# Optimization experiments

Measured on AMD Instinct MI355X. Metric: run time of the kernel, lower is better.

The kernel has to match this reference:

```python
import math
import jax, jax.numpy as jnp
import numpy as np

DIM = 384
NUM_HEADS = 12
KS = 7
GROUP_WIDTH = 8
LAM = 1.0
GAMMA = 1.0
DIM_QK = DIM // 3 * 2  # 256, multiple of group_width
DIM_V = DIM
SCALE = (DIM // NUM_HEADS) ** -0.5
GROUPS = DIM_QK // GROUP_WIDTH  # 32


def setup_inputs() -> dict:
    key = jax.random.key(0)
    ks = jax.random.split(key, 10)
    B_, N = 32, 196
    x = jax.random.normal(ks[0], (B_, N, DIM), dtype=jnp.float32)
    qkv_out = DIM_QK * 2 + DIM_V  # 704
    w_qkv = jax.random.normal(ks[1], (qkv_out, DIM), dtype=jnp.float32) * 0.02
    b_qkv = jnp.zeros((qkv_out,), dtype=jnp.float32)
    # grouped 7x7 conv: (out=DIM_QK, in_per_group=GROUP_WIDTH, KS, KS)
    w_dw = jax.random.normal(ks[2], (DIM_QK, GROUP_WIDTH, KS, KS), dtype=jnp.float32) * 0.05
    b_dw = jnp.zeros((DIM_QK,), dtype=jnp.float32)
    # 1x1 conv to KS^2 * num_heads channels
    w_pw = jax.random.normal(ks[3], (KS * KS * NUM_HEADS, DIM_QK), dtype=jnp.float32) * 0.05
    b_pw = jnp.zeros((KS * KS * NUM_HEADS,), dtype=jnp.float32)
    # ghost head: cat(ghost_mul ~ randn, ghost_add ~ trunc_normal(0.02)) -> (2,1,DIM_V,KS,KS)
    ghost_mul = jax.random.normal(ks[4], (1, 1, DIM_V, KS, KS), dtype=jnp.float32)
    ghost_add = jax.random.normal(ks[5], (1, 1, DIM_V, KS, KS), dtype=jnp.float32) * 0.02
    ghost_head = jnp.concatenate((ghost_mul, ghost_add), axis=0)
    w_proj = jax.random.normal(ks[6], (DIM, DIM_V), dtype=jnp.float32) * 0.02
    b_proj = jnp.zeros((DIM,), dtype=jnp.float32)
    return {"x": x, "w_qkv": w_qkv, "b_qkv": b_qkv, "w_dw": w_dw, "b_dw": b_dw,
            "w_pw": w_pw, "b_pw": b_pw, "ghost_head": ghost_head,
            "w_proj": w_proj, "b_proj": b_proj}


def reference(x, w_qkv, b_qkv, w_dw, b_dw, w_pw, b_pw, ghost_head, w_proj, b_proj):
    B, N, C = x.shape
    H = W = int(math.sqrt(N))
    G, Cg, ks = NUM_HEADS, DIM_V // NUM_HEADS, KS

    qkv = jnp.einsum('bnc,oc->bno', x, w_qkv) + b_qkv
    q, k, v = jnp.split(qkv, (DIM_QK, 2 * DIM_QK), axis=-1)
    q = jnp.transpose(q, (0, 2, 1)).reshape(B, DIM_QK, H, W)
    k = jnp.transpose(k, (0, 2, 1)).reshape(B, DIM_QK, H, W)
    v = jnp.transpose(v, (0, 2, 1)).reshape(B, DIM_V, H, W)

    # Hadamard QK interaction + attention-map generator
    hp = q * k * SCALE
    pad = ks // 2
    h = jax.lax.conv_general_dilated(
        hp, w_dw, window_strides=(1, 1), padding=((pad, pad), (pad, pad)),
        feature_group_count=GROUPS, dimension_numbers=('NCHW', 'OIHW', 'NCHW'))
    h = h + b_dw[None, :, None, None]
    h = jax.nn.gelu(h, approximate=False)
    h = jnp.einsum('bchw,oc->bohw', h, w_pw) + b_pw[None, :, None, None]  # (B, ks^2*G, H, W)

    h_attn = jax.nn.softmax(h.reshape(B * G, ks * ks, H, W), axis=1)
    v_g = v.reshape(B * G, Cg, H, W)

    # ghost heads (broadcast over batch, split channels into heads)
    gh = jnp.broadcast_to(ghost_head, (2, B, DIM_V, ks, ks)).reshape(2, B * G, Cg, ks * ks)
    ghost_mul = gh[0] ** LAM        # (BG, Cg, ks^2)
    ghost_add = gh[1] * GAMMA       # (BG, Cg, ks^2)

    # elsa_op: windowed weighted sum (unfold equivalent, torch channel-major order)
    vp = jnp.pad(v_g, ((0, 0), (0, 0), (pad, pad), (pad, pad)))
    patches = jnp.stack([vp[:, :, i:i + H, j:j + W]
                         for i in range(ks) for j in range(ks)], axis=2)  # (BG, Cg, ks^2, H, W)
    filt = (ghost_mul[:, :, :, None, None] * h_attn[:, None, :, :, :]
            + ghost_add[:, :, :, None, None])
    out = (patches * filt).sum(axis=2)  # (BG, Cg, H, W)

    out = out.reshape(B, DIM_V, H, W).transpose(0, 2, 3, 1).reshape(B, N, DIM_V)
    y = jnp.einsum('bnc,oc->bno', out, w_proj) + b_proj
    return y
```

## Files before the change

### kernel.cpp

```cpp
#include <hip/hip_runtime.h>
#include <hip/hip_bf16.h>

#define B_    32
#define N_    196
#define H_    14
#define DIMC  384
#define DQK   256
#define DV    384
#define NH    12
#define CG    32
#define NPW   588
#define PAD_  3
#define SCALE_ 0.17677669529663687f

typedef __bf16 bf16x8 __attribute__((ext_vector_type(8)));
typedef float  f32x4  __attribute__((ext_vector_type(4)));

__device__ inline bf16x8 bf16x8_zero() {
    bf16x8 z;
    #pragma unroll
    for (int j = 0; j < 8; ++j) z[j] = (__bf16)0.0f;
    return z;
}

__device__ inline void split2(float v, __hip_bfloat16& h, __hip_bfloat16& l) {
    h = __float2bfloat16(v);
    l = __float2bfloat16(v - __bfloat162float(h));
}

__global__ __launch_bounds__(256) void k_split(
    const float* __restrict__ s0, const float* __restrict__ s1,
    const float* __restrict__ s2, const float* __restrict__ s3,
    __hip_bfloat16* __restrict__ h0, __hip_bfloat16* __restrict__ l0,
    __hip_bfloat16* __restrict__ h1, __hip_bfloat16* __restrict__ l1,
    __hip_bfloat16* __restrict__ h2, __hip_bfloat16* __restrict__ l2,
    __hip_bfloat16* __restrict__ h3, __hip_bfloat16* __restrict__ l3)
{
    int i = blockIdx.x * 256 + threadIdx.x;
    if (i >= 762624) return;
    const float* src; __hip_bfloat16 *dh, *dl; int off;
    if      (i < 602112) { src = s0; dh = h0; dl = l0; off = i; }
    else if (i < 688128) { src = s1; dh = h1; dl = l1; off = i - 602112; }
    else if (i < 725760) { src = s2; dh = h2; dl = l2; off = i - 688128; }
    else                 { src = s3; dh = h3; dl = l3; off = i - 725760; }
    const float4 v = ((const float4*)src)[off];
    union { __hip_bfloat16 b[4]; uint2 u; } H, L;
    split2(v.x, H.b[0], L.b[0]); split2(v.y, H.b[1], L.b[1]);
    split2(v.z, H.b[2], L.b[2]); split2(v.w, H.b[3], L.b[3]);
    ((uint2*)dh)[off] = H.u;
    ((uint2*)dl)[off] = L.u;
}

template<int EPI>
__global__ __launch_bounds__(256) void k_mfma(
    const __hip_bfloat16* __restrict__ Phi, const __hip_bfloat16* __restrict__ Plo,
    const __hip_bfloat16* __restrict__ Qhi, const __hip_bfloat16* __restrict__ Qlo,
    const float* __restrict__ bias, int K, int nQ,
    float* __restrict__ out0, float* __restrict__ out1, float* __restrict__ out2)
{
    __shared__ ushort lds[16384];
    const int t    = threadIdx.x;
    const int m0   = blockIdx.x * 128;
    const int n0   = blockIdx.y * 128;
    const int lane = t & 63;
    const int wv   = t >> 6;
    const int wm   = (wv >> 1) * 64;
    const int wn   = (wv & 1) * 64;
    const int l16  = lane & 15;
    const int kb   = lane >> 4;

    f32x4 acc[4][4];
    #pragma unroll
    for (int mi = 0; mi < 4; ++mi)
        #pragma unroll
        for (int nj = 0; nj < 4; ++nj) acc[mi][nj] = f32x4{0.f, 0.f, 0.f, 0.f};

    for (int k0 = 0; k0 < K; k0 += 32) {
        bf16x8 rA[2][2], rB[2][2];
        #pragma unroll
        for (int q = 0; q < 2; ++q) {
            const int u = q * 256 + t;
            const int r = u >> 2;
            const int kk = (u & 3) * 8;
            const size_t pOff = (size_t)(m0 + r) * K + k0 + kk;
            rA[q][0] = *(const bf16x8*)(Phi + pOff);
            rA[q][1] = *(const bf16x8*)(Plo + pOff);
            if (n0 + r < nQ) {
                const size_t qOff = (size_t)(n0 + r) * K + k0 + kk;
                rB[q][0] = *(const bf16x8*)(Qhi + qOff);
                rB[q][1] = *(const bf16x8*)(Qlo + qOff);
            } else { rB[q][0] = bf16x8_zero(); rB[q][1] = bf16x8_zero(); }
        }
        __syncthreads();
        #pragma unroll
        for (int q = 0; q < 2; ++q) {
            const int u  = q * 256 + t;
            const int r  = u >> 2;
            const int sw = ((u << 4) ^ ((r & 7) << 4)) >> 1;
            *(bf16x8*)&lds[sw]         = rA[q][0];
            *(bf16x8*)&lds[sw + 4096]  = rA[q][1];
            *(bf16x8*)&lds[sw + 8192]  = rB[q][0];
            *(bf16x8*)&lds[sw + 12288] = rB[q][1];
        }
        __syncthreads();
        bf16x8 bh[4], bl[4];
        #pragma unroll
        for (int nj = 0; nj < 4; ++nj) {
            const int br  = wn + nj * 16 + l16;
            const int idx = ((br * 64 + kb * 16) ^ ((br & 7) << 4)) >> 1;
            bh[nj] = *(const bf16x8*)&lds[8192 + idx];
            bl[nj] = *(const bf16x8*)&lds[12288 + idx];
        }
        #pragma unroll
        for (int mi = 0; mi < 4; ++mi) {
            const int ar  = wm + mi * 16 + l16;
            const int idx = ((ar * 64 + kb * 16) ^ ((ar & 7) << 4)) >> 1;
            const bf16x8 ah = *(const bf16x8*)&lds[idx];
            const bf16x8 al = *(const bf16x8*)&lds[4096 + idx];
            #pragma unroll
            for (int nj = 0; nj < 4; ++nj) {
                acc[mi][nj] = __builtin_amdgcn_mfma_f32_16x16x32_bf16(ah, bh[nj], acc[mi][nj], 0, 0, 0);
                acc[mi][nj] = __builtin_amdgcn_mfma_f32_16x16x32_bf16(ah, bl[nj], acc[mi][nj], 0, 0, 0);
                acc[mi][nj] = __builtin_amdgcn_mfma_f32_16x16x32_bf16(al, bh[nj], acc[mi][nj], 0, 0, 0);
            }
        }
    }

    #pragma unroll
    for (int mi = 0; mi < 4; ++mi) {
        #pragma unroll
        for (int r = 0; r < 4; ++r) {
            const int m = m0 + wm + mi * 16 + kb * 4 + r;
            #pragma unroll
            for (int nj = 0; nj < 4; ++nj) {
                const int col = n0 + wn + nj * 16 + l16;
                const float v = acc[mi][nj][r];
                if (EPI == 0) {
                    const float val = v + bias[col];
                    const int bb = m / N_, n = m - bb * N_;
                    if (col < DQK)          out0[((size_t)bb * DQK + col) * N_ + n] = val;
                    else if (col < 2*DQK)   out1[((size_t)bb * DQK + (col - DQK)) * N_ + n] = val;
                    else                    out2[((size_t)bb * DV + (col - 2*DQK)) * N_ + n] = val;
                } else if (EPI == 1) {
                    if (col < NPW) out0[(size_t)m * NPW + col] = v + bias[col];
                } else {
                    out0[(size_t)m * DV + col] = v + bias[col];
                }
            }
        }
    }
}

__global__ __launch_bounds__(256) void k_dwconv(const float* __restrict__ qT,
    const float* __restrict__ kT, const float* __restrict__ w_dw,
    const float* __restrict__ b_dw,
    __hip_bfloat16* __restrict__ h1t_hi, __hip_bfloat16* __restrict__ h1t_lo)
{
    const int b  = blockIdx.x;
    const int gp = blockIdx.y;
    __shared__ float hp[16 * 400];
    __shared__ float wsm[16 * 392];
    const int t = threadIdx.x;
    for (int i = t; i < 16 * 400; i += 256) hp[i] = 0.f;
    for (int i = t; i < 16 * 392; i += 256) wsm[i] = w_dw[gp * 6272 + i];
    __syncthreads();
    for (int i = t; i < 16 * N_; i += 256) {
        const int cl = i / N_;
        const int n  = i - cl * N_;
        const int y  = n / H_, x = n - y * H_;
        const size_t gi = ((size_t)b * DQK + gp * 16 + cl) * N_ + n;
        hp[cl * 400 + (y + PAD_) * 20 + (x + PAD_)] = qT[gi] * kT[gi] * SCALE_;
    }
    __syncthreads();
    if (t < 224) {
        const int od = t / 14;
        const int y  = t - od * 14;
        const int icb = (od >> 3) << 3;
        float acc[14];
        #pragma unroll
        for (int x = 0; x < 14; ++x) acc[x] = 0.f;
        for (int ic = 0; ic < 8; ++ic) {
            const float* hrow = &hp[(icb + ic) * 400];
            const float* wrow = &wsm[od * 392 + ic * 49];
            #pragma unroll
            for (int ky = 0; ky < 7; ++ky) {
                float r[20];
                #pragma unroll
                for (int ii = 0; ii < 20; ii += 4)
                    *(float4*)&r[ii] = *(const float4*)&hrow[(y + ky) * 20 + ii];
                #pragma unroll
                for (int kx = 0; kx < 7; ++kx) {
                    const float wv = wrow[ky * 7 + kx];
                    #pragma unroll
                    for (int x = 0; x < 14; ++x)
                        acc[x] += r[x + kx] * wv;
                }
            }
        }
        const float bv = b_dw[gp * 16 + od];
        const int c = gp * 16 + od;
        #pragma unroll
        for (int x = 0; x < 14; ++x) {
            const float s  = acc[x] + bv;
            const float gv = 0.5f * s * (1.f + erff(s * 0.70710678118654752440f));
            __hip_bfloat16 hb, lb; split2(gv, hb, lb);
            const size_t o = ((size_t)b * N_ + y * H_ + x) * DQK + c;
            h1t_hi[o] = hb; h1t_lo[o] = lb;
        }
    }
}

__global__ __launch_bounds__(256) void k_elsa(const float* __restrict__ h2t,
    const float* __restrict__ vT, const float* __restrict__ ghost,
    __hip_bfloat16* __restrict__ orm_hi, __hip_bfloat16* __restrict__ orm_lo)
{
    const int b = blockIdx.x;
    const int g = blockIdx.y;
    __shared__ float attn[49 * N_];
    __shared__ float vp[8 * 401];
    __shared__ float gm[8 * 49];
    __shared__ float ga[8 * 49];
    const int t = threadIdx.x;

    const float* src = h2t + (size_t)b * N_ * NPW + g * 49;
    for (int i = t; i < 49 * N_; i += 256) {
        const int n = i / 49, p = i - n * 49;
        attn[p * N_ + n] = src[(size_t)n * NPW + p];
    }
    __syncthreads();

    if (t < N_) {
        float mx = -1e30f;
        for (int p = 0; p < 49; ++p) mx = fmaxf(mx, attn[p * N_ + t]);
        float s = 0.f;
        for (int p = 0; p < 49; ++p) {
            const float e = expf(attn[p * N_ + t] - mx);
            attn[p * N_ + t] = e;
            s += e;
        }
        const float inv = 1.f / s;
        for (int p = 0; p < 49; ++p) attn[p * N_ + t] *= inv;
    }
    __syncthreads();

    for (int cc = 0; cc < 4; ++cc) {
        const int c0 = cc * 8;
        for (int i = t; i < 8 * 401; i += 256) vp[i] = 0.f;
        for (int i = t; i < 8 * 49; i += 256) {
            gm[i] = ghost[(size_t)(g * CG + c0) * 49 + i];
            ga[i] = ghost[(size_t)DV * 49 + (g * CG + c0) * 49 + i];
        }
        __syncthreads();
        for (int i = t; i < 8 * N_; i += 256) {
            const int c = i / N_;
            const int n = i - c * N_;
            const int y = n / H_, x = n - y * H_;
            vp[c * 401 + (y + PAD_) * 20 + (x + PAD_)] =
                vT[((size_t)b * DV + g * CG + c0 + c) * N_ + n];
        }
        __syncthreads();

        for (int idx = t; idx < 8 * N_; idx += 256) {
            const int c = idx & 7;
            const int n = idx >> 3;
            const int y = n / H_, x = n - y * H_;
            const float* vrow = &vp[c * 401];
            const float* gmr  = &gm[c * 49];
            const float* gar  = &ga[c * 49];
            float s = 0.f;
            #pragma unroll
            for (int ky = 0; ky < 7; ++ky)
                #pragma unroll
                for (int kx = 0; kx < 7; ++kx) {
                    const int p = ky * 7 + kx;
                    s += vrow[(y + ky) * 20 + (x + kx)]
                       * (gmr[p] * attn[p * N_ + n] + gar[p]);
                }
            __hip_bfloat16 hb, lb; split2(s, hb, lb);
            const size_t o = ((size_t)b * N_ + n) * DV + g * CG + c0 + c;
            orm_hi[o] = hb; orm_lo[o] = lb;
        }
        __syncthreads();
    }
}

extern "C" void kernel_launch(void* const* d_in, const int* in_sizes, int n_in,
                              void* d_out, int out_size, void* d_ws, size_t ws_size,
                              hipStream_t stream)
{
    const float* x      = (const float*)d_in[0];
    const float* w_qkv  = (const float*)d_in[1];
    const float* b_qkv  = (const float*)d_in[2];
    const float* w_dw   = (const float*)d_in[3];
    const float* b_dw   = (const float*)d_in[4];
    const float* w_pw   = (const float*)d_in[5];
    const float* b_pw   = (const float*)d_in[6];
    const float* ghost  = (const float*)d_in[7];
    const float* w_proj = (const float*)d_in[8];
    const float* b_proj = (const float*)d_in[9];
    float* y  = (float*)d_out;
    char* ws = (char*)d_ws;

    __hip_bfloat16* x_hi     = (__hip_bfloat16*)(ws + 0);
    __hip_bfloat16* x_lo     = (__hip_bfloat16*)(ws + 4816896);
    __hip_bfloat16* wqkv_hi  = (__hip_bfloat16*)(ws + 9633792);
    __hip_bfloat16* wqkv_lo  = (__hip_bfloat16*)(ws + 10321920);
    float*          h2t      = (float*)         (ws + 0);
    float*          qT       = (float*)         (ws + 14751744);
    float*          kT       = (float*)         (ws + 21174272);
    __hip_bfloat16* orm_hi   = (__hip_bfloat16*)(ws + 14751744);
    __hip_bfloat16* orm_lo   = (__hip_bfloat16*)(ws + 19568640);
    float*          vT       = (float*)         (ws + 27596800);
    __hip_bfloat16* wpw_hi   = (__hip_bfloat16*)(ws + 37230592);
    __hip_bfloat16* wpw_lo   = (__hip_bfloat16*)(ws + 37531648);
    __hip_bfloat16* wproj_hi = (__hip_bfloat16*)(ws + 37832704);
    __hip_bfloat16* wproj_lo = (__hip_bfloat16*)(ws + 38127616);
    __hip_bfloat16* h1t_hi   = (__hip_bfloat16*)(ws + 38422528);
    __hip_bfloat16* h1t_lo   = (__hip_bfloat16*)(ws + 41633792);

    k_split<<<2979, 256, 0, stream>>>(x, w_qkv, w_pw, w_proj,
        x_hi, x_lo, wqkv_hi, wqkv_lo, wpw_hi, wpw_lo, wproj_hi, wproj_lo);

    k_mfma<0><<<dim3(49, 7), 256, 0, stream>>>(x_hi, x_lo, wqkv_hi, wqkv_lo,
        b_qkv, DIMC, 896, qT, kT, vT);

    k_dwconv<<<dim3(32, 16), 256, 0, stream>>>(qT, kT, w_dw, b_dw, h1t_hi, h1t_lo);

    k_mfma<1><<<dim3(49, 5), 256, 0, stream>>>(h1t_hi, h1t_lo, wpw_hi, wpw_lo,
        b_pw, DQK, NPW, h2t, nullptr, nullptr);

    k_elsa<<<dim3(32, 12), 256, 0, stream>>>(h2t, vT, ghost, orm_hi, orm_lo);

    k_mfma<2><<<dim3(49, 3), 256, 0, stream>>>(orm_hi, orm_lo, wproj_hi, wproj_lo,
        b_proj, DV, DV, y, nullptr, nullptr);
}
```

Measured before the change: 260.0 us.

## Split ELSA kernel across channel chunks and keep softmax attention in registers

The ELSA kernel is now launched with a third grid dimension over the four 8-channel chunks, so four times as many blocks run and each handles only one chunk. Every thread owns one spatial position, loads its 49 attention logits straight from global memory, runs the softmax in registers and reuses those values across the 8 channels. This drops the large shared-memory attention transpose and several barriers, which should raise occupancy. The cost is that the softmax is recomputed once per chunk, each thread needs many more registers, and 60 of 256 threads sit idle.

Result: faster. 241.9 us (-7.0%).

```diff
diff --git a/kernel.cpp b/kernel.cpp
--- a/kernel.cpp
+++ b/kernel.cpp
@@ -214,73 +214,65 @@
     const float* __restrict__ vT, const float* __restrict__ ghost,
     __hip_bfloat16* __restrict__ orm_hi, __hip_bfloat16* __restrict__ orm_lo)
 {
-    const int b = blockIdx.x;
-    const int g = blockIdx.y;
-    __shared__ float attn[49 * N_];
-    __shared__ float vp[8 * 401];
-    __shared__ float gm[8 * 49];
-    __shared__ float ga[8 * 49];
+    const int b  = blockIdx.x;
+    const int g  = blockIdx.y;
+    const int c0 = blockIdx.z * 8;
+    __shared__ float vp[8 * 400];
+    __shared__ float gmga[8 * 49 * 2];
     const int t = threadIdx.x;
 
-    const float* src = h2t + (size_t)b * N_ * NPW + g * 49;
-    for (int i = t; i < 49 * N_; i += 256) {
-        const int n = i / 49, p = i - n * 49;
-        attn[p * N_ + n] = src[(size_t)n * NPW + p];
+    for (int i = t; i < 8 * 400; i += 256) vp[i] = 0.f;
+    for (int i = t; i < 8 * 49; i += 256) {
+        const int c = i / 49, p = i - c * 49;
+        gmga[(c * 49 + p) * 2 + 0] = ghost[(size_t)(g * CG + c0 + c) * 49 + p];
+        gmga[(c * 49 + p) * 2 + 1] = ghost[(size_t)DV * 49 + (g * CG + c0 + c) * 49 + p];
     }
     __syncthreads();
+    for (int i = t; i < 8 * N_; i += 256) {
+        const int c = i / N_;
+        const int n = i - c * N_;
+        const int y = n / H_, x = n - y * H_;
+        vp[c * 400 + (y + PAD_) * 20 + (x + PAD_)] =
+            vT[((size_t)b * DV + g * CG + c0 + c) * N_ + n];
+    }
+    __syncthreads();
 
     if (t < N_) {
+        const int n = t;
+        const int y = n / H_, x = n - y * H_;
+        const int base = y * 20 + x;
+        const size_t m = (size_t)b * N_ + n;
+
+        const float* hr = h2t + m * NPW + g * 49;
+        float a[49];
+        #pragma unroll
+        for (int p = 0; p < 49; ++p) a[p] = hr[p];
         float mx = -1e30f;
-        for (int p = 0; p < 49; ++p) mx = fmaxf(mx, attn[p * N_ + t]);
-        float s = 0.f;
-        for (int p = 0; p < 49; ++p) {
-            const float e = expf(attn[p * N_ + t] - mx);
-            attn[p * N_ + t] = e;
-            s += e;
-        }
-        const float inv = 1.f / s;
-        for (int p = 0; p < 49; ++p) attn[p * N_ + t] *= inv;
-    }
-    __syncthreads();
-
-    for (int cc = 0; cc < 4; ++cc) {
-        const int c0 = cc * 8;
-        for (int i = t; i < 8 * 401; i += 256) vp[i] = 0.f;
-        for (int i = t; i < 8 * 49; i += 256) {
-            gm[i] = ghost[(size_t)(g * CG + c0) * 49 + i];
-            ga[i] = ghost[(size_t)DV * 49 + (g * CG + c0) * 49 + i];
-        }
-        __syncthreads();
-        for (int i = t; i < 8 * N_; i += 256) {
-            const int c = i / N_;
-            const int n = i - c * N_;
-            const int y = n / H_, x = n - y * H_;
-            vp[c * 401 + (y + PAD_) * 20 + (x + PAD_)] =
-                vT[((size_t)b * DV + g * CG + c0 + c) * N_ + n];
-        }
-        __syncthreads();
-
-        for (int idx = t; idx < 8 * N_; idx += 256) {
-            const int c = idx & 7;
-            const int n = idx >> 3;
-            const int y = n / H_, x = n - y * H_;
-            const float* vrow = &vp[c * 401];
-            const float* gmr  = &gm[c * 49];
-            const float* gar  = &ga[c * 49];
+        #pragma unroll
+        for (int p = 0; p < 49; ++p) mx = fmaxf(mx, a[p]);
+        float ssum = 0.f;
+        #pragma unroll
+        for (int p = 0; p < 49; ++p) { a[p] = expf(a[p] - mx); ssum += a[p]; }
+        const float inv = 1.f / ssum;
+        #pragma unroll
+        for (int p = 0; p < 49; ++p) a[p] *= inv;
+
+        #pragma unroll 1
+        for (int c = 0; c < 8; ++c) {
+            const float* vrow = &vp[c * 400 + base];
+            const float* gg   = &gmga[c * 98];
             float s = 0.f;
             #pragma unroll
             for (int ky = 0; ky < 7; ++ky)
                 #pragma unroll
                 for (int kx = 0; kx < 7; ++kx) {
                     const int p = ky * 7 + kx;
-                    s += vrow[(y + ky) * 20 + (x + kx)]
-                       * (gmr[p] * attn[p * N_ + n] + gar[p]);
+                    s += vrow[ky * 20 + kx] * (gg[p * 2] * a[p] + gg[p * 2 + 1]);
                 }
             __hip_bfloat16 hb, lb; split2(s, hb, lb);
-            const size_t o = ((size_t)b * N_ + n) * DV + g * CG + c0 + c;
+            const size_t o = m * DV + g * CG + c0 + c;
             orm_hi[o] = hb; orm_lo[o] = lb;
         }
-        __syncthreads();
     }
 }
 
@@ -329,7 +321,7 @@
     k_mfma<1><<<dim3(49, 5), 256, 0, stream>>>(h1t_hi, h1t_lo, wpw_hi, wpw_lo,
         b_pw, DQK, NPW, h2t, nullptr, nullptr);
 
-    k_elsa<<<dim3(32, 12), 256, 0, stream>>>(h2t, vT, ghost, orm_hi, orm_lo);
+    k_elsa<<<dim3(32, 12, 4), 256, 0, stream>>>(h2t, vT, ghost, orm_hi, orm_lo);
 
     k_mfma<2><<<dim3(49, 3), 256, 0, stream>>>(orm_hi, orm_lo, wproj_hi, wproj_lo,
         b_proj, DV, DV, y, nullptr, nullptr);
```
